# Performance work log

Measured on AMD Instinct MI355X. Metric: run time of the kernel, lower is better.

## Reference

```python
import jax, jax.numpy as jnp
import numpy as np

T, B, C, H, W = 4, 8, 256, 56, 56
HEADS = 8
D_NORM = 8.0
LAMDA = 1
CV = C * LAMDA
EPS = 1e-5


def quant_if(x, D):
    # Q_IFNode with Quant surrogate: integer spike counts clip(round(x),0,D),
    # straight-through gradient = 1 on [0, D].
    y = jnp.clip(jnp.round(x), 0.0, D)
    mask = ((x >= 0.0) & (x <= D)).astype(x.dtype)
    return x * mask + jax.lax.stop_gradient(y - x * mask)


def conv_bn(x, w, p):
    # 1x1 conv (pointwise channel mix) fused with eval-mode BatchNorm.
    # x: [T,B,Cin,H,W], w: [Cout,Cin], p: [4,Cout]=(gamma,beta,mean,var)
    y = jnp.einsum('oc,tbchw->tbohw', w, x)
    gamma, beta, mean, var = p[0], p[1], p[2], p[3]
    s = gamma / jnp.sqrt(var + EPS)
    return y * s[None, None, :, None, None] + (beta - mean * s)[None, None, :, None, None]


def _to_heads(t, c):
    # [T,B,c,H,W] -> [T,B,HEADS,N,c//HEADS]  (channel split h-outer, matches torch reshape)
    return t.reshape(T, B, HEADS, c // HEADS, H * W).transpose(0, 1, 2, 4, 3)


def setup_inputs():
    key = jax.random.key(0)
    ks = jax.random.split(key, 9)

    def bn_params(k, c):
        k1, k2, k3, k4 = jax.random.split(k, 4)
        return jnp.stack([
            jax.random.uniform(k1, (c,)) + 0.5,        # gamma
            jax.random.normal(k2, (c,)) * 0.1,          # beta
            jax.random.normal(k3, (c,)) * 0.1,          # running mean
            jax.random.uniform(k4, (c,)) + 0.5,         # running var
        ]).astype(jnp.float32)

    x = jax.random.normal(ks[0], (T, B, C, H, W), dtype=jnp.float32)
    w_scale = 1.0 / np.sqrt(C)
    return {
        'x': x,
        'qw': jax.random.normal(ks[1], (C, C), dtype=jnp.float32) * w_scale,
        'qbn': bn_params(ks[2], C),
        'kw': jax.random.normal(ks[3], (C, C), dtype=jnp.float32) * w_scale,
        'kbn': bn_params(ks[4], C),
        'vw': jax.random.normal(ks[5], (CV, C), dtype=jnp.float32) * w_scale,
        'vbn': bn_params(ks[6], CV),
        'pw': jax.random.normal(ks[7], (C, CV), dtype=jnp.float32) * w_scale,
        'pbn': bn_params(ks[8], C),
    }


def reference(x, qw, qbn, kw, kbn, vw, vbn, pw, pbn):
    dh = C // HEADS
    scale = dh ** (-0.5)

    xs = quant_if(x, D_NORM) / D_NORM                       # head_spike / D_Norm
    q = conv_bn(xs, qw, qbn)
    k = conv_bn(xs, kw, kbn)
    v = conv_bn(xs, vw, vbn)

    qh = _to_heads(quant_if(q, D_NORM) / D_NORM, C)         # [T,B,h,N,dh]
    kh = _to_heads(quant_if(k, D_NORM) / D_NORM, C)
    vh = _to_heads(quant_if(v, D_NORM) / D_NORM, CV)        # [T,B,h,N,dv]

    # Softmax-free linear attention: (q @ k^T) @ v == q @ (k^T @ v), O(N*d^2).
    kv = jnp.einsum('tbhnd,tbhne->tbhde', kh, vh)            # [T,B,h,dh,dv]
    o = jnp.einsum('tbhnd,tbhde->tbhne', qh, kv) * (scale * 2.0)

    # [T,B,h,N,dv] -> [T,B,CV,N]
    o = o.transpose(0, 1, 2, 4, 3).reshape(T, B, CV, H * W)
    o = quant_if(o, D_NORM) / D_NORM                         # attn_spike / D_Norm
    o = o.reshape(T, B, CV, H, W)
    out = conv_bn(o, pw, pbn)                                # [T,B,C,H,W]
    return out
```

## Files before the change

### kernel.cpp

```cpp
#include <hip/hip_runtime.h>
#include <stdint.h>

#define TB_ 32
#define C_ 256
#define N_ 3136
#define TBC (C_ * N_)
#define ACT_SZ (TB_ * TBC)
#define XSB_TB 819200
#define PARTS 7
#define CHUNK 448

typedef __attribute__((ext_vector_type(8))) short bf16x8;
typedef __attribute__((ext_vector_type(4))) float f32x4;

__device__ __forceinline__ void glds16(const void* gp, void* lp) {
  __builtin_amdgcn_global_load_lds(
      (const __attribute__((address_space(1))) unsigned int*)gp,
      (__attribute__((address_space(3))) unsigned int*)lp, 16, 0, 0);
}

__device__ __forceinline__ unsigned short bf16rn(float f, float* val) {
  unsigned b = __float_as_uint(f);
  unsigned r = (b + 0x7fffu + ((b >> 16) & 1u)) >> 16;
  *val = __uint_as_float(r << 16);
  return (unsigned short)r;
}

__device__ __forceinline__ int dot4u(unsigned a, unsigned b, int c) {
  c += (int)(a & 255u)         * (int)(b & 255u);
  c += (int)((a >> 8) & 255u)  * (int)((b >> 8) & 255u);
  c += (int)((a >> 16) & 255u) * (int)((b >> 16) & 255u);
  c += (int)(a >> 24)          * (int)(b >> 24);
  return c;
}

__device__ __forceinline__ int dot4(unsigned a, unsigned b, int c) {
#if defined(__has_builtin)
#if __has_builtin(__builtin_amdgcn_sdot4)
  return __builtin_amdgcn_sdot4((int)a, (int)b, c, false);
#else
  return dot4u(a, b, c);
#endif
#else
  return dot4u(a, b, c);
#endif
}

__global__ __launch_bounds__(256) void prep_all(
    const float* __restrict__ qbn, const float* __restrict__ kbn,
    const float* __restrict__ vbn, const float* __restrict__ pbn,
    const float* __restrict__ qw, const float* __restrict__ kw,
    const float* __restrict__ vw, const float* __restrict__ pw,
    float* __restrict__ bnw, unsigned short* __restrict__ wsp,
    int* __restrict__ kvg) {
  const int bx = blockIdx.x;
  const int t = threadIdx.x;
  if (bx == 0) {
    const float* ps[4] = {qbn, kbn, vbn, pbn};
#pragma unroll
    for (int i = 0; i < 4; ++i) {
      const float* p = ps[i];
      float g = p[t], be = p[256 + t], mn = p[512 + t], vr = p[768 + t];
      float s = g / sqrtf(vr + 1e-5f);
      float b = __fsub_rn(be, __fmul_rn(mn, s));
      bnw[i * 512 + t] = s;
      bnw[i * 512 + 256 + t] = b;
    }
  } else if (bx <= 1024) {
    const float* Ws[4] = {qw, kw, vw, pw};
    int id = bx - 1, co = id & 255, m = id >> 8;
    float w = Ws[m][co * 256 + t];
    float h1, h2, h3r;
    unsigned short u1 = bf16rn(w, &h1);
    float r1 = __fsub_rn(w, h1);
    unsigned short u2 = bf16rn(r1, &h2);
    float r2 = __fsub_rn(r1, h2);
    unsigned short u3 = bf16rn(r2, &h3r);
    int rt = co >> 7, ks = t >> 5;
    int lane = (co & 15) + 16 * ((t >> 3) & 3);
    unsigned short us[3] = {u1, u2, u3};
#pragma unroll
    for (int sp = 0; sp < 3; ++sp) {
      size_t off = (size_t)((((m * 3 + sp) * 2 + rt) * 8 + ks)) * 4096 + lane * 8 + (t & 7);
      wsp[off] = us[sp];
    }
  } else {
    int tb = bx - 1025;
    int4* p = (int4*)(kvg + (size_t)tb * 8192);
    for (int i = t; i < 2048; i += 256) p[i] = make_int4(0, 0, 0, 0);
  }
}

__global__ __launch_bounds__(256) void quant_x_t(const float* __restrict__ x,
                                                 unsigned short* __restrict__ xsb) {
  __shared__ unsigned short s[64 * 68];
  const int t = threadIdx.x;
  const int n0 = blockIdx.x * 64;
  const int tb = blockIdx.y;
  const float* X = x + (size_t)tb * TBC;
  const int nl = t & 63, cq = t >> 6;
  const int c16 = t >> 4, p4 = (t & 15) * 4;

  unsigned short* dstb = xsb + (size_t)tb * XSB_TB;
  for (int cb = 0; cb < 4; ++cb) {
    int cbase = cb * 64;
#pragma unroll
    for (int i = 0; i < 4; ++i) {
      int c = i * 16 + c16;
      float4 v = *(const float4*)&X[(size_t)(cbase + c) * N_ + n0 + p4];
      unsigned short r0 = (unsigned short)(__float_as_uint(fminf(fmaxf(rintf(v.x), 0.f), 8.f)) >> 16);
      unsigned short r1 = (unsigned short)(__float_as_uint(fminf(fmaxf(rintf(v.y), 0.f), 8.f)) >> 16);
      unsigned short r2 = (unsigned short)(__float_as_uint(fminf(fmaxf(rintf(v.z), 0.f), 8.f)) >> 16);
      unsigned short r3 = (unsigned short)(__float_as_uint(fminf(fmaxf(rintf(v.w), 0.f), 8.f)) >> 16);
      uint2 pk2;
      pk2.x = (unsigned)r0 | ((unsigned)r1 << 16);
      pk2.y = (unsigned)r2 | ((unsigned)r3 << 16);
      *(uint2*)&s[c * 68 + p4] = pk2;
    }
    __syncthreads();
#pragma unroll 2
    for (int j = 0; j < 2; ++j) {
      int ccl = j * 4 + cq;
      int cc = cb * 8 + ccl;
      unsigned short v8[8];
#pragma unroll
      for (int d = 0; d < 8; ++d) v8[d] = s[(ccl * 8 + d) * 68 + nl];
      int n = n0 + nl;
      uint4 pk;
      pk.x = (unsigned)v8[0] | ((unsigned)v8[1] << 16);
      pk.y = (unsigned)v8[2] | ((unsigned)v8[3] << 16);
      pk.z = (unsigned)v8[4] | ((unsigned)v8[5] << 16);
      pk.w = (unsigned)v8[6] | ((unsigned)v8[7] << 16);
      *(uint4*)&dstb[(size_t)(n >> 4) * 4096 + cc * 128 + (n & 15) * 8] = pk;
    }
    __syncthreads();
  }
}

__global__ __launch_bounds__(256) void qkv_mfma_sw(
    const unsigned short* __restrict__ xsb, const unsigned short* __restrict__ wsp,
    const float* __restrict__ bnw,
    uint8_t* __restrict__ qsb, uint8_t* __restrict__ ks_, uint8_t* __restrict__ vs) {
  __shared__ __align__(16) char smem[32768];
  char* smA = smem;
  char* smB = smem + 16384;
  const int t = threadIdx.x;
  const int L = t & 63, w = t >> 6;
  const int wrow = w >> 1, wcol = w & 1;
  const int b = blockIdx.x;
  const int oct = b / 48, rem = b % 48;
  const int s = rem >> 3, gl = rem & 7;
  const int g = oct * 8 + gl;
  const int ntile = g % 25, tb = g / 25;
  const int conv = s >> 1, rt = s & 1;
  const int n0 = ntile * 128;

  const char* Bb = (const char*)(xsb + (size_t)tb * XSB_TB) + (size_t)ntile * 65536;
  const char* Ab = (const char*)wsp + ((size_t)(conv * 3) * 16 + rt * 8) * 8192;

  f32x4 acc[4][4];
#pragma unroll
  for (int i = 0; i < 4; ++i)
#pragma unroll
    for (int j = 0; j < 4; ++j) acc[i][j] = (f32x4){0.f, 0.f, 0.f, 0.f};

  glds16(Ab + t * 16, smA + t * 16);
  glds16(Ab + t * 16 + 4096, smA + t * 16 + 4096);
  glds16(Bb + (size_t)w * 8192 + L * 16, smB + t * 16);
  glds16(Bb + (size_t)(w + 4) * 8192 + L * 16, smB + t * 16 + 4096);
  __syncthreads();

#pragma unroll 1
  for (int st = 0; st < 24; ++st) {
    const int cur = (st & 1) << 13;
    const int nxt = 8192 - cur;
    const int s1 = st + 1;
    if (s1 < 24) {
      const char* An = Ab + (size_t)(((s1 >> 3) * 16) + (s1 & 7)) * 8192;
      glds16(An + t * 16, smA + nxt + t * 16);
      glds16(An + t * 16 + 4096, smA + nxt + t * 16 + 4096);
      const char* Bk = Bb + (size_t)(s1 & 7) * 1024;
      glds16(Bk + (size_t)w * 8192 + L * 16, smB + nxt + t * 16);
      glds16(Bk + (size_t)(w + 4) * 8192 + L * 16, smB + nxt + t * 16 + 4096);
    }
    bf16x8 af[4], bfr[4];
#pragma unroll
    for (int i = 0; i < 4; ++i) {
      af[i] = *(const bf16x8*)(smA + cur + (wrow * 4 + i) * 1024 + L * 16);
      bfr[i] = *(const bf16x8*)(smB + cur + (wcol * 4 + i) * 1024 + L * 16);
    }
#pragma unroll
    for (int i = 0; i < 4; ++i)
#pragma unroll
      for (int j = 0; j < 4; ++j)
        acc[i][j] = __builtin_amdgcn_mfma_f32_16x16x32_bf16(af[i], bfr[j], acc[i][j], 0, 0, 0);
    __syncthreads();
  }

  const float* sbn = bnw + conv * 512;
  const int rbase = rt * 128;
  if (conv == 0) {
    uint8_t* qtb = qsb + (size_t)tb * XSB_TB;
#pragma unroll
    for (int i = 0; i < 4; ++i) {
      int co0 = rbase + wrow * 64 + i * 16 + ((L >> 4) << 2);
      float s0 = sbn[co0], b0 = sbn[256 + co0];
      float s1 = sbn[co0 + 1], b1 = sbn[256 + co0 + 1];
      float s2 = sbn[co0 + 2], b2 = sbn[256 + co0 + 2];
      float s3 = sbn[co0 + 3], b3 = sbn[256 + co0 + 3];
#pragma unroll
      for (int j = 0; j < 4; ++j) {
        int n = n0 + wcol * 64 + j * 16 + (L & 15);
        if (n < N_) {
          float ss[4] = {s0, s1, s2, s3}, bb[4] = {b0, b1, b2, b3};
          unsigned wb = 0;
#pragma unroll
          for (int r = 0; r < 4; ++r) {
            float y = acc[i][j][r] * 0.125f;
            float tt = __fadd_rn(__fmul_rn(y, ss[r]), bb[r]);
            float rr = fminf(fmaxf(rintf(tt), 0.f), 8.f);
            wb |= ((unsigned)(uint8_t)rr) << (8 * r);
          }
          *(unsigned*)&qtb[(size_t)(n >> 4) * 4096 + (co0 >> 3) * 128 + (n & 15) * 8 + (co0 & 7)] = wb;
        }
      }
    }
  } else {
    uint8_t* outp = (conv == 1 ? ks_ : vs) + (size_t)tb * TBC;
#pragma unroll
    for (int i = 0; i < 4; ++i) {
      int co0 = rbase + wrow * 64 + i * 16 + ((L >> 4) << 2);
#pragma unroll
      for (int j = 0; j < 4; ++j) {
        int n = n0 + wcol * 64 + j * 16 + (L & 15);
        if (n < N_) {
#pragma unroll
          for (int r = 0; r < 4; ++r) {
            int co = co0 + r;
            float y = acc[i][j][r] * 0.125f;
            float tt = __fadd_rn(__fmul_rn(y, sbn[co]), sbn[256 + co]);
            float rr = fminf(fmaxf(rintf(tt), 0.f), 8.f);
            outp[(size_t)co * N_ + n] = (uint8_t)rr;
          }
        }
      }
    }
  }
}

__global__ __launch_bounds__(256) void attn_kv(
    const uint8_t* __restrict__ ks, const uint8_t* __restrict__ vs,
    int* __restrict__ kvg) {
  const int h = blockIdx.x, tb = blockIdx.y, part = blockIdx.z;
  const int tid = threadIdx.x;
  __shared__ unsigned sk[32][68];
  __shared__ unsigned sv[32][68];
  const uint8_t* K = ks + (size_t)tb * TBC + h * 32 * N_;
  const uint8_t* V = vs + (size_t)tb * TBC + h * 32 * N_;
  const int d0 = (tid >> 4) * 2;
  const int e0 = (tid & 15) * 2;
  const int pbase = part * CHUNK;
  const int pend = pbase + CHUNK;
  int acc[2][2] = {};

  for (int nt = 0; nt < 2; ++nt) {
    int n0 = pbase + nt * 256;
    if (n0 >= pend) break;
    if (nt) __syncthreads();
#pragma unroll
    for (int i = 0; i < 8; ++i) {
      int idx = tid + i * 256;
      int d = idx >> 6, w2 = idx & 63;
      int n = n0 + w2 * 4;
      unsigned kw_ = 0, vw_ = 0;
      if (n < pend) {
        kw_ = *(const unsigned*)&K[d * N_ + n];
        vw_ = *(const unsigned*)&V[d * N_ + n];
      }
      sk[d][w2] = kw_;
      sv[d][w2] = vw_;
    }
    __syncthreads();
#pragma unroll
    for (int w2 = 0; w2 < 64; w2 += 4) {
      uint4 ka = *(const uint4*)&sk[d0][w2];
      uint4 kb = *(const uint4*)&sk[d0 + 1][w2];
      uint4 va = *(const uint4*)&sv[e0][w2];
      uint4 vb = *(const uint4*)&sv[e0 + 1][w2];
      unsigned kwds[2][4] = {{ka.x, ka.y, ka.z, ka.w}, {kb.x, kb.y, kb.z, kb.w}};
      unsigned vwds[2][4] = {{va.x, va.y, va.z, va.w}, {vb.x, vb.y, vb.z, vb.w}};
#pragma unroll
      for (int di = 0; di < 2; ++di)
#pragma unroll
        for (int ej = 0; ej < 2; ++ej)
#pragma unroll
          for (int c = 0; c < 4; ++c)
            acc[di][ej] = dot4(kwds[di][c], vwds[ej][c], acc[di][ej]);
    }
  }
  int* dst = kvg + ((size_t)(tb * 8 + h)) * 1024;
  atomicAdd(&dst[d0 * 32 + e0], acc[0][0]);
  atomicAdd(&dst[d0 * 32 + e0 + 1], acc[0][1]);
  atomicAdd(&dst[(d0 + 1) * 32 + e0], acc[1][0]);
  atomicAdd(&dst[(d0 + 1) * 32 + e0 + 1], acc[1][1]);
}

__global__ __launch_bounds__(256) void kv_finish(const int* __restrict__ kvg,
                                                 unsigned short* __restrict__ kvimg) {
  const int tb = blockIdx.x, t = threadIdx.x;
  const int* src = kvg + (size_t)tb * 8192;
  unsigned short* dst = kvimg + (size_t)tb * 24576;
#pragma unroll 4
  for (int i = 0; i < 32; ++i) {
    int idx = t + i * 256;
    int h = idx >> 10, rem = idx & 1023, d = rem >> 5, e = rem & 31;
    int v = src[idx];
    int b1 = (v > 0) ? (32 - __clz(v)) : 0;
    int sh1 = b1 > 8 ? b1 - 8 : 0;
    int hi = (v >> sh1) << sh1;
    int r1 = v - hi;
    int b2 = (r1 > 0) ? (32 - __clz(r1)) : 0;
    int sh2 = b2 > 8 ? b2 - 8 : 0;
    int mid = (r1 >> sh2) << sh2;
    int r2 = r1 - mid;
    int parts[3] = {hi, mid, r2};
    int mtile = e >> 4, lane = (e & 15) + 16 * (d >> 3), j = d & 7;
#pragma unroll
    for (int sp = 0; sp < 3; ++sp) {
      float f = (float)parts[sp];
      dst[(size_t)h * 3072 + (sp * 2 + mtile) * 512 + lane * 8 + j] =
          (unsigned short)(__float_as_uint(f) >> 16);
    }
  }
}

__global__ __launch_bounds__(256) void attn_o_mfma(
    const uint8_t* __restrict__ qsb, const unsigned short* __restrict__ kvimg,
    unsigned short* __restrict__ osb) {
  __shared__ __align__(16) char smem[14336];
  char* smB = smem;
  char* smA = smem + 8192;
  const int t = threadIdx.x;
  const int L = t & 63, wv = t >> 6;
  const int b = blockIdx.x;
  const int ntile = b % 25, tb = b / 25;
  const uint8_t* Q = qsb + (size_t)tb * XSB_TB + (size_t)ntile * 8 * 4096;
  const unsigned short* KV = kvimg + (size_t)tb * 24576;
  unsigned short* osb_tb = osb + (size_t)tb * XSB_TB;
  const float cscale = (float)(0.3535533905932738 / 512.0);

#pragma unroll 1
  for (int h = 0; h < 8; ++h) {
    __syncthreads();
    const char* Ah = (const char*)(KV + (size_t)h * 3072);
    glds16(Ah + t * 16, smA + t * 16);
    if (t < 128) glds16(Ah + 4096 + t * 16, smA + 4096 + t * 16);
#pragma unroll
    for (int it = 0; it < 4; ++it) {
      int w2 = t + it * 256;
      int gl2 = w2 >> 7;
      int wl = w2 & 127;
      int ccp = wl >> 5;
      int rem = (w2 * 4) & 127;
      int n16 = rem >> 3, k7b = rem & 7;
      unsigned wd = *(const unsigned*)&Q[(size_t)gl2 * 4096 + (h * 4 + ccp) * 128 + n16 * 8 + k7b];
      unsigned short* ds = (unsigned short*)smB + gl2 * 512 + (ccp * 16 + n16) * 8 + k7b;
      float f0 = (float)(wd & 255u), f1 = (float)((wd >> 8) & 255u);
      float f2 = (float)((wd >> 16) & 255u), f3 = (float)(wd >> 24);
      uint2 pk;
      pk.x = (__float_as_uint(f0) >> 16) | ((__float_as_uint(f1) >> 16) << 16);
      pk.y = (__float_as_uint(f2) >> 16) | ((__float_as_uint(f3) >> 16) << 16);
      *(uint2*)ds = pk;
    }
    __syncthreads();
    bf16x8 bfr[2];
#pragma unroll
    for (int jj = 0; jj < 2; ++jj)
      bfr[jj] = *(const bf16x8*)(smB + (wv * 2 + jj) * 1024 + L * 16);
    f32x4 acc[2][2];
#pragma unroll
    for (int i = 0; i < 2; ++i)
#pragma unroll
      for (int jj = 0; jj < 2; ++jj) acc[i][jj] = (f32x4){0.f, 0.f, 0.f, 0.f};
#pragma unroll
    for (int sp = 0; sp < 3; ++sp) {
      bf16x8 a0 = *(const bf16x8*)(smA + (sp * 2 + 0) * 1024 + L * 16);
      bf16x8 a1 = *(const bf16x8*)(smA + (sp * 2 + 1) * 1024 + L * 16);
#pragma unroll
      for (int jj = 0; jj < 2; ++jj) {
        acc[0][jj] = __builtin_amdgcn_mfma_f32_16x16x32_bf16(a0, bfr[jj], acc[0][jj], 0, 0, 0);
        acc[1][jj] = __builtin_amdgcn_mfma_f32_16x16x32_bf16(a1, bfr[jj], acc[1][jj], 0, 0, 0);
      }
    }
#pragma unroll
    for (int i = 0; i < 2; ++i) {
      int c0 = h * 32 + i * 16 + ((L >> 4) << 2);
#pragma unroll
      for (int jj = 0; jj < 2; ++jj) {
        int n = ntile * 128 + (wv * 2 + jj) * 16 + (L & 15);
        if (n < N_) {
          unsigned short u[4];
#pragma unroll
          for (int r = 0; r < 4; ++r) {
            float of = acc[i][jj][r] * cscale;
            float rr = fminf(fmaxf(rintf(of), 0.f), 8.f);
            u[r] = (unsigned short)(__float_as_uint(rr) >> 16);
          }
          uint2 pk;
          pk.x = (unsigned)u[0] | ((unsigned)u[1] << 16);
          pk.y = (unsigned)u[2] | ((unsigned)u[3] << 16);
          *(uint2*)&osb_tb[(size_t)(n >> 4) * 4096 + (c0 >> 3) * 128 + (n & 15) * 8 + (c0 & 7)] = pk;
        }
      }
    }
  }
}

__global__ __launch_bounds__(256) void out_mfma_sw(
    const unsigned short* __restrict__ osb, const unsigned short* __restrict__ wsp,
    const float* __restrict__ bnw, float* __restrict__ out) {
  __shared__ __align__(16) char smem[32768];
  char* smA = smem;
  char* smB = smem + 16384;
  const int t = threadIdx.x;
  const int L = t & 63, w = t >> 6;
  const int wrow = w >> 1, wcol = w & 1;
  const int b = blockIdx.x;
  const int oct = b / 16, rem = b % 16;
  const int rt = rem >> 3, gl = rem & 7;
  const int g = oct * 8 + gl;
  const int ntile = g % 25, tb = g / 25;
  const int n0 = ntile * 128;
  const char* Bb = (const char*)(osb + (size_t)tb * XSB_TB) + (size_t)ntile * 65536;
  const char* Ab = (const char*)wsp + ((size_t)9 * 16 + rt * 8) * 8192;

  f32x4 acc[4][4];
#pragma unroll
  for (int i = 0; i < 4; ++i)
#pragma unroll
    for (int j = 0; j < 4; ++j) acc[i][j] = (f32x4){0.f, 0.f, 0.f, 0.f};

  glds16(Ab + t * 16, smA + t * 16);
  glds16(Ab + t * 16 + 4096, smA + t * 16 + 4096);
  glds16(Bb + (size_t)w * 8192 + L * 16, smB + t * 16);
  glds16(Bb + (size_t)(w + 4) * 8192 + L * 16, smB + t * 16 + 4096);
  __syncthreads();

#pragma unroll 1
  for (int st = 0; st < 16; ++st) {
    const int cur = (st & 1) << 13;
    const int nxt = 8192 - cur;
    const int s1 = st + 1;
    if (s1 < 16) {
      const char* An = Ab + (size_t)(((s1 >> 3) * 16) + (s1 & 7)) * 8192;
      glds16(An + t * 16, smA + nxt + t * 16);
      glds16(An + t * 16 + 4096, smA + nxt + t * 16 + 4096);
      const char* Bk = Bb + (size_t)(s1 & 7) * 1024;
      glds16(Bk + (size_t)w * 8192 + L * 16, smB + nxt + t * 16);
      glds16(Bk + (size_t)(w + 4) * 8192 + L * 16, smB + nxt + t * 16 + 4096);
    }
    bf16x8 af[4], bfr[4];
#pragma unroll
    for (int i = 0; i < 4; ++i) {
      af[i] = *(const bf16x8*)(smA + cur + (wrow * 4 + i) * 1024 + L * 16);
      bfr[i] = *(const bf16x8*)(smB + cur + (wcol * 4 + i) * 1024 + L * 16);
    }
#pragma unroll
    for (int i = 0; i < 4; ++i)
#pragma unroll
      for (int j = 0; j < 4; ++j)
        acc[i][j] = __builtin_amdgcn_mfma_f32_16x16x32_bf16(af[i], bfr[j], acc[i][j], 0, 0, 0);
    __syncthreads();
  }

  float* O = out + (size_t)tb * TBC;
  const float* sbn = bnw + 3 * 512;
  const int rbase = rt * 128;
#pragma unroll
  for (int i = 0; i < 4; ++i) {
    int co0 = rbase + wrow * 64 + i * 16 + ((L >> 4) << 2);
#pragma unroll
    for (int j = 0; j < 4; ++j) {
      int n = n0 + wcol * 64 + j * 16 + (L & 15);
      if (n < N_) {
#pragma unroll
        for (int r = 0; r < 4; ++r) {
          int co = co0 + r;
          float y = acc[i][j][r] * 0.125f;
          O[(size_t)co * N_ + n] = __fadd_rn(__fmul_rn(y, sbn[co]), sbn[256 + co]);
        }
      }
    }
  }
}

extern "C" void kernel_launch(void* const* d_in, const int* in_sizes, int n_in,
                              void* d_out, int out_size, void* d_ws, size_t ws_size,
                              hipStream_t stream) {
  const float* x   = (const float*)d_in[0];
  const float* qw  = (const float*)d_in[1];
  const float* qbn = (const float*)d_in[2];
  const float* kw  = (const float*)d_in[3];
  const float* kbn = (const float*)d_in[4];
  const float* vw  = (const float*)d_in[5];
  const float* vbn = (const float*)d_in[6];
  const float* pw  = (const float*)d_in[7];
  const float* pbn = (const float*)d_in[8];
  float* out = (float*)d_out;

  uint8_t* ws = (uint8_t*)d_ws;
  float* bnw           = (float*)ws;
  unsigned short* wsp  = (unsigned short*)(ws + 8192);
  unsigned short* xsb  = (unsigned short*)(ws + 1581056);
  uint8_t* qsb         = ws + 54009856;
  uint8_t* ksp         = ws + 80224256;
  uint8_t* vsp         = ws + 105914368;
  int* kvg             = (int*)(ws + 131604480);
  unsigned short* kvimg = (unsigned short*)(ws + 132653056);
  unsigned short* osb  = xsb;

  prep_all<<<1057, 256, 0, stream>>>(qbn, kbn, vbn, pbn, qw, kw, vw, pw, bnw, wsp, kvg);
  quant_x_t<<<dim3(49, 32), 256, 0, stream>>>(x, xsb);
  qkv_mfma_sw<<<4800, 256, 0, stream>>>(xsb, wsp, bnw, qsb, ksp, vsp);
  attn_kv<<<dim3(8, 32, PARTS), 256, 0, stream>>>(ksp, vsp, kvg);
  kv_finish<<<32, 256, 0, stream>>>(kvg, kvimg);
  attn_o_mfma<<<800, 256, 0, stream>>>(qsb, kvimg, osb);
  out_mfma_sw<<<1600, 256, 0, stream>>>(osb, wsp, bnw, out);
}
```

Measured before the change: 418.0 us.

## Load weight fragments directly to registers and triple-buffer B with one barrier per step

In both MFMA GEMM kernels the weight (A) fragments are now loaded from global memory straight into registers and prefetched one step ahead, instead of being staged through LDS. The activation (B) tiles use a three-slot LDS ring with explicit vmcnt waits and a single s_barrier per iteration, where before there was a double buffer with two syncthreads. This is meant to cut LDS traffic and barrier count and to shrink LDS per block so occupancy can rise. In exchange it adds register pressure from the prefetched A fragments, and correctness now depends on the hand-counted vmcnt values.

```diff
diff --git a/kernel.cpp b/kernel.cpp
--- a/kernel.cpp
+++ b/kernel.cpp
@@ -141,9 +141,7 @@
     const unsigned short* __restrict__ xsb, const unsigned short* __restrict__ wsp,
     const float* __restrict__ bnw,
     uint8_t* __restrict__ qsb, uint8_t* __restrict__ ks_, uint8_t* __restrict__ vs) {
-  __shared__ __align__(16) char smem[32768];
-  char* smA = smem;
-  char* smB = smem + 16384;
+  __shared__ __align__(16) char smem[24576];
   const int t = threadIdx.x;
   const int L = t & 63, w = t >> 6;
   const int wrow = w >> 1, wcol = w & 1;
@@ -156,7 +154,8 @@
   const int n0 = ntile * 128;
 
   const char* Bb = (const char*)(xsb + (size_t)tb * XSB_TB) + (size_t)ntile * 65536;
-  const char* Ab = (const char*)wsp + ((size_t)(conv * 3) * 16 + rt * 8) * 8192;
+  const char* Ab = (const char*)wsp + ((size_t)(conv * 3) * 16 + rt * 8) * 8192
+                   + (size_t)(wrow * 4) * 1024 + (size_t)L * 16;
 
   f32x4 acc[4][4];
 #pragma unroll
@@ -164,37 +163,40 @@
 #pragma unroll
     for (int j = 0; j < 4; ++j) acc[i][j] = (f32x4){0.f, 0.f, 0.f, 0.f};
 
-  glds16(Ab + t * 16, smA + t * 16);
-  glds16(Ab + t * 16 + 4096, smA + t * 16 + 4096);
-  glds16(Bb + (size_t)w * 8192 + L * 16, smB + t * 16);
-  glds16(Bb + (size_t)(w + 4) * 8192 + L * 16, smB + t * 16 + 4096);
-  __syncthreads();
+  glds16(Bb + (size_t)w * 8192 + L * 16, smem + t * 16);
+  glds16(Bb + (size_t)(w + 4) * 8192 + L * 16, smem + t * 16 + 4096);
+  bf16x8 a_cur[4], a_nxt[4];
+#pragma unroll
+  for (int i = 0; i < 4; ++i) a_cur[i] = *(const bf16x8*)(Ab + i * 1024);
 
 #pragma unroll 1
   for (int st = 0; st < 24; ++st) {
-    const int cur = (st & 1) << 13;
-    const int nxt = 8192 - cur;
-    const int s1 = st + 1;
-    if (s1 < 24) {
+    char* bufc = smem + (st % 3) * 8192;
+    if (st < 23) {
+      const int s1 = st + 1;
+      char* bufn = smem + (s1 % 3) * 8192;
+      const char* Bk = Bb + (size_t)(s1 & 7) * 1024;
+      glds16(Bk + (size_t)w * 8192 + L * 16, bufn + t * 16);
+      glds16(Bk + (size_t)(w + 4) * 8192 + L * 16, bufn + t * 16 + 4096);
       const char* An = Ab + (size_t)(((s1 >> 3) * 16) + (s1 & 7)) * 8192;
-      glds16(An + t * 16, smA + nxt + t * 16);
-      glds16(An + t * 16 + 4096, smA + nxt + t * 16 + 4096);
-      const char* Bk = Bb + (size_t)(s1 & 7) * 1024;
-      glds16(Bk + (size_t)w * 8192 + L * 16, smB + nxt + t * 16);
-      glds16(Bk + (size_t)(w + 4) * 8192 + L * 16, smB + nxt + t * 16 + 4096);
-    }
-    bf16x8 af[4], bfr[4];
-#pragma unroll
-    for (int i = 0; i < 4; ++i) {
-      af[i] = *(const bf16x8*)(smA + cur + (wrow * 4 + i) * 1024 + L * 16);
-      bfr[i] = *(const bf16x8*)(smB + cur + (wcol * 4 + i) * 1024 + L * 16);
-    }
+#pragma unroll
+      for (int i = 0; i < 4; ++i) a_nxt[i] = *(const bf16x8*)(An + i * 1024);
+      asm volatile("s_waitcnt vmcnt(6)" ::: "memory");
+    } else {
+      asm volatile("s_waitcnt vmcnt(0)" ::: "memory");
+    }
+    __builtin_amdgcn_s_barrier();
+    bf16x8 bfr[4];
 #pragma unroll
     for (int i = 0; i < 4; ++i)
+      bfr[i] = *(const bf16x8*)(bufc + (wcol * 4 + i) * 1024 + L * 16);
+#pragma unroll
+    for (int i = 0; i < 4; ++i)
 #pragma unroll
       for (int j = 0; j < 4; ++j)
-        acc[i][j] = __builtin_amdgcn_mfma_f32_16x16x32_bf16(af[i], bfr[j], acc[i][j], 0, 0, 0);
-    __syncthreads();
+        acc[i][j] = __builtin_amdgcn_mfma_f32_16x16x32_bf16(a_cur[i], bfr[j], acc[i][j], 0, 0, 0);
+#pragma unroll
+    for (int i = 0; i < 4; ++i) a_cur[i] = a_nxt[i];
   }
 
   const float* sbn = bnw + conv * 512;
@@ -419,9 +421,7 @@
 __global__ __launch_bounds__(256) void out_mfma_sw(
     const unsigned short* __restrict__ osb, const unsigned short* __restrict__ wsp,
     const float* __restrict__ bnw, float* __restrict__ out) {
-  __shared__ __align__(16) char smem[32768];
-  char* smA = smem;
-  char* smB = smem + 16384;
+  __shared__ __align__(16) char smem[24576];
   const int t = threadIdx.x;
   const int L = t & 63, w = t >> 6;
   const int wrow = w >> 1, wcol = w & 1;
@@ -432,7 +432,8 @@
   const int ntile = g % 25, tb = g / 25;
   const int n0 = ntile * 128;
   const char* Bb = (const char*)(osb + (size_t)tb * XSB_TB) + (size_t)ntile * 65536;
-  const char* Ab = (const char*)wsp + ((size_t)9 * 16 + rt * 8) * 8192;
+  const char* Ab = (const char*)wsp + ((size_t)9 * 16 + rt * 8) * 8192
+                   + (size_t)(wrow * 4) * 1024 + (size_t)L * 16;
 
   f32x4 acc[4][4];
 #pragma unroll
@@ -440,37 +441,40 @@
 #pragma unroll
     for (int j = 0; j < 4; ++j) acc[i][j] = (f32x4){0.f, 0.f, 0.f, 0.f};
 
-  glds16(Ab + t * 16, smA + t * 16);
-  glds16(Ab + t * 16 + 4096, smA + t * 16 + 4096);
-  glds16(Bb + (size_t)w * 8192 + L * 16, smB + t * 16);
-  glds16(Bb + (size_t)(w + 4) * 8192 + L * 16, smB + t * 16 + 4096);
-  __syncthreads();
+  glds16(Bb + (size_t)w * 8192 + L * 16, smem + t * 16);
+  glds16(Bb + (size_t)(w + 4) * 8192 + L * 16, smem + t * 16 + 4096);
+  bf16x8 a_cur[4], a_nxt[4];
+#pragma unroll
+  for (int i = 0; i < 4; ++i) a_cur[i] = *(const bf16x8*)(Ab + i * 1024);
 
 #pragma unroll 1
   for (int st = 0; st < 16; ++st) {
-    const int cur = (st & 1) << 13;
-    const int nxt = 8192 - cur;
-    const int s1 = st + 1;
-    if (s1 < 16) {
+    char* bufc = smem + (st % 3) * 8192;
+    if (st < 15) {
+      const int s1 = st + 1;
+      char* bufn = smem + (s1 % 3) * 8192;
+      const char* Bk = Bb + (size_t)(s1 & 7) * 1024;
+      glds16(Bk + (size_t)w * 8192 + L * 16, bufn + t * 16);
+      glds16(Bk + (size_t)(w + 4) * 8192 + L * 16, bufn + t * 16 + 4096);
       const char* An = Ab + (size_t)(((s1 >> 3) * 16) + (s1 & 7)) * 8192;
-      glds16(An + t * 16, smA + nxt + t * 16);
-      glds16(An + t * 16 + 4096, smA + nxt + t * 16 + 4096);
-      const char* Bk = Bb + (size_t)(s1 & 7) * 1024;
-      glds16(Bk + (size_t)w * 8192 + L * 16, smB + nxt + t * 16);
-      glds16(Bk + (size_t)(w + 4) * 8192 + L * 16, smB + nxt + t * 16 + 4096);
-    }
-    bf16x8 af[4], bfr[4];
-#pragma unroll
-    for (int i = 0; i < 4; ++i) {
-      af[i] = *(const bf16x8*)(smA + cur + (wrow * 4 + i) * 1024 + L * 16);
-      bfr[i] = *(const bf16x8*)(smB + cur + (wcol * 4 + i) * 1024 + L * 16);
-    }
+#pragma unroll
+      for (int i = 0; i < 4; ++i) a_nxt[i] = *(const bf16x8*)(An + i * 1024);
+      asm volatile("s_waitcnt vmcnt(6)" ::: "memory");
+    } else {
+      asm volatile("s_waitcnt vmcnt(0)" ::: "memory");
+    }
+    __builtin_amdgcn_s_barrier();
+    bf16x8 bfr[4];
 #pragma unroll
     for (int i = 0; i < 4; ++i)
+      bfr[i] = *(const bf16x8*)(bufc + (wcol * 4 + i) * 1024 + L * 16);
+#pragma unroll
+    for (int i = 0; i < 4; ++i)
 #pragma unroll
       for (int j = 0; j < 4; ++j)
-        acc[i][j] = __builtin_amdgcn_mfma_f32_16x16x32_bf16(af[i], bfr[j], acc[i][j], 0, 0, 0);
-    __syncthreads();
+        acc[i][j] = __builtin_amdgcn_mfma_f32_16x16x32_bf16(a_cur[i], bfr[j], acc[i][j], 0, 0, 0);
+#pragma unroll
+    for (int i = 0; i < 4; ++i) a_cur[i] = a_nxt[i];
   }
 
   float* O = out + (size_t)tb * TBC;
```

Result: slower. 464.9 us (+11.2%).

## Triple-buffer LDS in QKV and output GEMMs with one barrier per stage

Applied to the files above, without the earlier changes.

Both MFMA GEMM kernels move from a double-buffered LDS ring with two syncthreads per stage to a three-slot ring. Each stage waits with a partial vmcnt and passes one raw s_barrier. The next tile's global-to-LDS loads can stay in flight while the current tile is read, which removes the trailing barrier and the full drain of outstanding loads. LDS per block grows from 32KB to 48KB, which may reduce how many blocks fit on each CU, and correctness now depends on hand-written waitcnt counts and on the three-slot reuse distance.

```diff
diff --git a/kernel.cpp b/kernel.cpp
--- a/kernel.cpp
+++ b/kernel.cpp
@@ -141,9 +141,7 @@
     const unsigned short* __restrict__ xsb, const unsigned short* __restrict__ wsp,
     const float* __restrict__ bnw,
     uint8_t* __restrict__ qsb, uint8_t* __restrict__ ks_, uint8_t* __restrict__ vs) {
-  __shared__ __align__(16) char smem[32768];
-  char* smA = smem;
-  char* smB = smem + 16384;
+  __shared__ __align__(16) char smem[49152];
   const int t = threadIdx.x;
   const int L = t & 63, w = t >> 6;
   const int wrow = w >> 1, wcol = w & 1;
@@ -164,37 +162,39 @@
 #pragma unroll
     for (int j = 0; j < 4; ++j) acc[i][j] = (f32x4){0.f, 0.f, 0.f, 0.f};
 
-  glds16(Ab + t * 16, smA + t * 16);
-  glds16(Ab + t * 16 + 4096, smA + t * 16 + 4096);
-  glds16(Bb + (size_t)w * 8192 + L * 16, smB + t * 16);
-  glds16(Bb + (size_t)(w + 4) * 8192 + L * 16, smB + t * 16 + 4096);
-  __syncthreads();
+  glds16(Ab + t * 16, smem + t * 16);
+  glds16(Ab + t * 16 + 4096, smem + t * 16 + 4096);
+  glds16(Bb + (size_t)w * 8192 + L * 16, smem + 8192 + t * 16);
+  glds16(Bb + (size_t)(w + 4) * 8192 + L * 16, smem + 8192 + t * 16 + 4096);
 
 #pragma unroll 1
   for (int st = 0; st < 24; ++st) {
-    const int cur = (st & 1) << 13;
-    const int nxt = 8192 - cur;
-    const int s1 = st + 1;
-    if (s1 < 24) {
-      const char* An = Ab + (size_t)(((s1 >> 3) * 16) + (s1 & 7)) * 8192;
-      glds16(An + t * 16, smA + nxt + t * 16);
-      glds16(An + t * 16 + 4096, smA + nxt + t * 16 + 4096);
+    char* slotc = smem + (st % 3) * 16384;
+    if (st < 23) {
+      const int s1 = st + 1;
+      char* slotn = smem + (s1 % 3) * 16384;
+      const char* Ak = Ab + (size_t)(((s1 >> 3) * 16) + (s1 & 7)) * 8192;
+      glds16(Ak + t * 16, slotn + t * 16);
+      glds16(Ak + t * 16 + 4096, slotn + t * 16 + 4096);
       const char* Bk = Bb + (size_t)(s1 & 7) * 1024;
-      glds16(Bk + (size_t)w * 8192 + L * 16, smB + nxt + t * 16);
-      glds16(Bk + (size_t)(w + 4) * 8192 + L * 16, smB + nxt + t * 16 + 4096);
-    }
+      glds16(Bk + (size_t)w * 8192 + L * 16, slotn + 8192 + t * 16);
+      glds16(Bk + (size_t)(w + 4) * 8192 + L * 16, slotn + 8192 + t * 16 + 4096);
+      asm volatile("s_waitcnt vmcnt(4)" ::: "memory");
+    } else {
+      asm volatile("s_waitcnt vmcnt(0)" ::: "memory");
+    }
+    __builtin_amdgcn_s_barrier();
     bf16x8 af[4], bfr[4];
 #pragma unroll
     for (int i = 0; i < 4; ++i) {
-      af[i] = *(const bf16x8*)(smA + cur + (wrow * 4 + i) * 1024 + L * 16);
-      bfr[i] = *(const bf16x8*)(smB + cur + (wcol * 4 + i) * 1024 + L * 16);
+      af[i] = *(const bf16x8*)(slotc + (wrow * 4 + i) * 1024 + L * 16);
+      bfr[i] = *(const bf16x8*)(slotc + 8192 + (wcol * 4 + i) * 1024 + L * 16);
     }
 #pragma unroll
     for (int i = 0; i < 4; ++i)
 #pragma unroll
       for (int j = 0; j < 4; ++j)
         acc[i][j] = __builtin_amdgcn_mfma_f32_16x16x32_bf16(af[i], bfr[j], acc[i][j], 0, 0, 0);
-    __syncthreads();
   }
 
   const float* sbn = bnw + conv * 512;
@@ -419,9 +419,7 @@
 __global__ __launch_bounds__(256) void out_mfma_sw(
     const unsigned short* __restrict__ osb, const unsigned short* __restrict__ wsp,
     const float* __restrict__ bnw, float* __restrict__ out) {
-  __shared__ __align__(16) char smem[32768];
-  char* smA = smem;
-  char* smB = smem + 16384;
+  __shared__ __align__(16) char smem[49152];
   const int t = threadIdx.x;
   const int L = t & 63, w = t >> 6;
   const int wrow = w >> 1, wcol = w & 1;
@@ -440,37 +438,39 @@
 #pragma unroll
     for (int j = 0; j < 4; ++j) acc[i][j] = (f32x4){0.f, 0.f, 0.f, 0.f};
 
-  glds16(Ab + t * 16, smA + t * 16);
-  glds16(Ab + t * 16 + 4096, smA + t * 16 + 4096);
-  glds16(Bb + (size_t)w * 8192 + L * 16, smB + t * 16);
-  glds16(Bb + (size_t)(w + 4) * 8192 + L * 16, smB + t * 16 + 4096);
-  __syncthreads();
+  glds16(Ab + t * 16, smem + t * 16);
+  glds16(Ab + t * 16 + 4096, smem + t * 16 + 4096);
+  glds16(Bb + (size_t)w * 8192 + L * 16, smem + 8192 + t * 16);
+  glds16(Bb + (size_t)(w + 4) * 8192 + L * 16, smem + 8192 + t * 16 + 4096);
 
 #pragma unroll 1
   for (int st = 0; st < 16; ++st) {
-    const int cur = (st & 1) << 13;
-    const int nxt = 8192 - cur;
-    const int s1 = st + 1;
-    if (s1 < 16) {
-      const char* An = Ab + (size_t)(((s1 >> 3) * 16) + (s1 & 7)) * 8192;
-      glds16(An + t * 16, smA + nxt + t * 16);
-      glds16(An + t * 16 + 4096, smA + nxt + t * 16 + 4096);
+    char* slotc = smem + (st % 3) * 16384;
+    if (st < 15) {
+      const int s1 = st + 1;
+      char* slotn = smem + (s1 % 3) * 16384;
+      const char* Ak = Ab + (size_t)(((s1 >> 3) * 16) + (s1 & 7)) * 8192;
+      glds16(Ak + t * 16, slotn + t * 16);
+      glds16(Ak + t * 16 + 4096, slotn + t * 16 + 4096);
       const char* Bk = Bb + (size_t)(s1 & 7) * 1024;
-      glds16(Bk + (size_t)w * 8192 + L * 16, smB + nxt + t * 16);
-      glds16(Bk + (size_t)(w + 4) * 8192 + L * 16, smB + nxt + t * 16 + 4096);
-    }
+      glds16(Bk + (size_t)w * 8192 + L * 16, slotn + 8192 + t * 16);
+      glds16(Bk + (size_t)(w + 4) * 8192 + L * 16, slotn + 8192 + t * 16 + 4096);
+      asm volatile("s_waitcnt vmcnt(4)" ::: "memory");
+    } else {
+      asm volatile("s_waitcnt vmcnt(0)" ::: "memory");
+    }
+    __builtin_amdgcn_s_barrier();
     bf16x8 af[4], bfr[4];
 #pragma unroll
     for (int i = 0; i < 4; ++i) {
-      af[i] = *(const bf16x8*)(smA + cur + (wrow * 4 + i) * 1024 + L * 16);
-      bfr[i] = *(const bf16x8*)(smB + cur + (wcol * 4 + i) * 1024 + L * 16);
+      af[i] = *(const bf16x8*)(slotc + (wrow * 4 + i) * 1024 + L * 16);
+      bfr[i] = *(const bf16x8*)(slotc + 8192 + (wcol * 4 + i) * 1024 + L * 16);
     }
 #pragma unroll
     for (int i = 0; i < 4; ++i)
 #pragma unroll
       for (int j = 0; j < 4; ++j)
         acc[i][j] = __builtin_amdgcn_mfma_f32_16x16x32_bf16(af[i], bfr[j], acc[i][j], 0, 0, 0);
-    __syncthreads();
   }
 
   float* O = out + (size_t)tb * TBC;
```

After: 394.7 us. -5.6%, faster.
